# Optimization experiments

Measured on AMD Instinct MI355X. Metric: run time of the kernel, lower is better.

The kernel has to match this reference:

```python
import jax, jax.numpy as jnp
import numpy as np

N_DNA = 220000   # multiple of 11 (11 pseudo-atoms per base-pair)
N_PROT = 120000
E = 1500000
C = 32           # prot_channels == dna_channels
IN = C + 4 + C   # [x_prot_j, ppf(4), x_dna_i]

BRANCH_MODS = [(0, 10), (1, 9), (2, 3, 4, 5), (6, 7, 8)]  # p, s, M, m edge groups


def setup_inputs() -> dict:
    key = jax.random.key(0)
    ks = jax.random.split(key, 10)
    return {
        "x_dna": jax.random.normal(ks[0], (N_DNA, C), jnp.float32),
        "v_dna": jax.random.normal(ks[1], (N_DNA, 3), jnp.float32),
        "x_prot": jax.random.normal(ks[2], (N_PROT, C), jnp.float32),
        "v_prot": jax.random.normal(ks[3], (N_PROT, 3), jnp.float32),
        "prot_vec": jax.random.normal(ks[4], (N_PROT, 3), jnp.float32),
        "dna_vec": jax.random.normal(ks[5], (N_DNA, 3), jnp.float32),
        "edge_src": jax.random.randint(ks[6], (E,), 0, N_PROT),
        "edge_dst": jax.random.randint(ks[7], (E,), 0, N_DNA),
        "W1": jax.random.normal(ks[8], (4, IN, C), jnp.float32) / np.sqrt(IN).astype(np.float32),
        "b1": jnp.zeros((4, C), jnp.float32),
        "W2": jax.random.normal(ks[9], (4, C, C), jnp.float32) / np.sqrt(C).astype(np.float32),
        "b2": jnp.zeros((4, C), jnp.float32),
    }


def _angle(v1, v2):
    cross = jnp.cross(v1, v2)
    return jnp.arctan2(jnp.linalg.norm(cross, axis=-1), jnp.sum(v1 * v2, axis=-1))


def _point_pair_features(pos_i, pos_j, n_i, n_j):
    d = pos_j - pos_i
    return jnp.stack([
        jnp.linalg.norm(d, axis=-1),
        _angle(n_i, d),
        _angle(n_j, d),
        _angle(n_i, n_j),
    ], axis=-1)  # [E, 4]


def reference(x_dna, v_dna, x_prot, v_prot, prot_vec, dna_vec,
              edge_src, edge_dst, W1, b1, W2, b2):
    n_dna, c = x_dna.shape
    # PPF: i = target (dna), j = source (prot)
    ppf = _point_pair_features(v_dna[edge_dst], v_prot[edge_src],
                               dna_vec[edge_dst], prot_vec[edge_src])
    # per-edge input features, add_target_features=True concatenates x_dna_i
    feat = jnp.concatenate([x_prot[edge_src], ppf, x_dna[edge_dst]], axis=-1)  # [E, IN]
    mod = edge_dst % 11
    out = jnp.zeros_like(x_dna)
    conv = jnp.zeros_like(x_dna)
    for b, mods in enumerate(BRANCH_MODS):
        mask = jnp.zeros(mod.shape, dtype=bool)
        for m in mods:
            mask = mask | (mod == m)
        h = jax.nn.relu(feat @ W1[b] + b1[b])
        h = jax.nn.relu(h @ W2[b] + b2[b])          # [E, C] per-edge messages
        agg = jax.ops.segment_sum(jnp.where(mask[:, None], h, 0.0),
                                  edge_dst, num_segments=n_dna)
        conv = conv + agg
        out = out + jax.nn.relu(agg)
    return out.reshape(-1, 11, c), conv
```

## Files before the change

### kernel.cpp

```cpp
#include <hip/hip_runtime.h>


#define IN_C 32
#define IN_F 68
#define TILE_A 4096
#define BK_SHIFT 9
#define NBKT_MAX 448
#define BCAP 6144

using bf16x8v = __attribute__((ext_vector_type(8))) short;
using f32x16v = __attribute__((ext_vector_type(16))) float;
using f32x2v  = __attribute__((ext_vector_type(2))) float;

union U4F { unsigned u[4]; bf16x8v v; };

__device__ __forceinline__ unsigned cvtpk_bf16(float a, float b) {
    unsigned r;
    asm("v_cvt_pk_bf16_f32 %0, %1, %2" : "=v"(r) : "v"(a), "v"(b));
    return r;
}
__device__ __forceinline__ float bflo(unsigned u) { return __uint_as_float(u << 16); }
__device__ __forceinline__ float bfhi(unsigned u) { return __uint_as_float(u & 0xffff0000u); }

__device__ __forceinline__ float angf(float ax, float ay, float az,
                                      float bx, float by, float bz) {
    float cx = ay * bz - az * by;
    float cy = az * bx - ax * bz;
    float cz = ax * by - ay * bx;
    float cn = sqrtf(cx * cx + cy * cy + cz * cz);
    float dt = ax * bx + ay * by + az * bz;
    return atan2f(cn, dt);
}

__device__ __forceinline__ int branch_of(int m) {
    if (m == 0 || m == 10) return 0;
    if (m == 1 || m == 9)  return 1;
    if (m >= 2 && m <= 5)  return 2;
    return 3;
}

__device__ __forceinline__ unsigned bf16r(float f) {
    unsigned u = __float_as_uint(f);
    return (u + 0x7fffu + ((u >> 16) & 1u)) >> 16;
}

__device__ __forceinline__ void precomp_body_fast(
    int t,
    const float* __restrict__ x_prot, const float* __restrict__ x_dna,
    const float* __restrict__ v_prot, const float* __restrict__ prot_vec,
    const float* __restrict__ v_dna, const float* __restrict__ dna_vec,
    const float* __restrict__ W1, const float* __restrict__ b1,
    int NP, int NPpad, int NB, int NBpad,
    unsigned* __restrict__ yrec, unsigned* __restrict__ drec)
{
    float h[IN_C];
    if (t < NPpad) {
        int p = t;
        if (p >= NP) return;
        float xs[IN_C];
        {
            const float4* xp = reinterpret_cast<const float4*>(x_prot + (size_t)p * IN_C);
            #pragma unroll
            for (int kk = 0; kk < 8; ++kk) {
                float4 xv = xp[kk];
                xs[4 * kk + 0] = xv.x; xs[4 * kk + 1] = xv.y;
                xs[4 * kk + 2] = xv.z; xs[4 * kk + 3] = xv.w;
            }
        }
        float vpx = v_prot[p * 3 + 0], vpy = v_prot[p * 3 + 1], vpz = v_prot[p * 3 + 2];
        float njx = prot_vec[p * 3 + 0], njy = prot_vec[p * 3 + 1], njz = prot_vec[p * 3 + 2];
        uint4 gr;
        gr.x = bf16r(vpx) | (bf16r(vpy) << 16);
        gr.y = bf16r(vpz) | (bf16r(njx) << 16);
        gr.z = bf16r(njy) | (bf16r(njz) << 16);
        gr.w = 0;
        #pragma unroll 1
        for (int g = 0; g < 4; ++g) {
            const float* Wa = W1 + g * (IN_F * IN_C);
            #pragma unroll
            for (int c = 0; c < IN_C; ++c) h[c] = 0.0f;
            #pragma unroll
            for (int k = 0; k < IN_C; ++k)
                #pragma unroll
                for (int c = 0; c < IN_C; ++c)
                    h[c] = fmaf(xs[k], Wa[k * IN_C + c], h[c]);
            unsigned yw[8];
            #pragma unroll
            for (int j = 0; j < 8; ++j) {
                int w = 0;
                w = __builtin_amdgcn_cvt_pk_fp8_f32(h[4 * j],     h[4 * j + 1], w, false);
                w = __builtin_amdgcn_cvt_pk_fp8_f32(h[4 * j + 2], h[4 * j + 3], w, true);
                yw[j] = (unsigned)w;
            }
            uint4* d4 = reinterpret_cast<uint4*>(yrec + ((size_t)g * NP + p) * 16);
            d4[0] = make_uint4(yw[0], yw[1], yw[2], yw[3]);
            d4[1] = make_uint4(yw[4], yw[5], yw[6], yw[7]);
            d4[2] = gr;
        }
    } else {
        int t2 = t - NPpad;
        int q = t2 / NBpad;
        if (q >= 11) return;
        int idx = t2 - q * NBpad;
        if (idx >= NB) return;
        int g, m;
        if (q < 2)      { g = 0; m = q ? 10 : 0; }
        else if (q < 4) { g = 1; m = (q == 2) ? 1 : 9; }
        else if (q < 8) { g = 2; m = 2 + (q - 4); }
        else            { g = 3; m = 6 + (q - 8); }
        int bb = __builtin_amdgcn_readfirstlane(g);
        int dn = idx * 11 + m;
        const float* Wa = W1 + bb * (IN_F * IN_C);
        const float* ba = b1 + bb * IN_C;
        #pragma unroll
        for (int c = 0; c < IN_C; ++c) h[c] = ba[c];
        const float4* xd = reinterpret_cast<const float4*>(x_dna + (size_t)dn * IN_C);
        #pragma unroll
        for (int kk = 0; kk < 8; ++kk) {
            float4 xv = xd[kk];
            float fs[4] = {xv.x, xv.y, xv.z, xv.w};
            #pragma unroll
            for (int j = 0; j < 4; ++j)
                #pragma unroll
                for (int c = 0; c < IN_C; ++c)
                    h[c] = fmaf(fs[j], Wa[(36 + kk * 4 + j) * IN_C + c], h[c]);
        }
        unsigned yw[16];
        #pragma unroll
        for (int j = 0; j < 16; ++j)
            yw[j] = bf16r(h[2 * j]) | (bf16r(h[2 * j + 1]) << 16);
        float vdx = v_dna[dn * 3 + 0], vdy = v_dna[dn * 3 + 1], vdz = v_dna[dn * 3 + 2];
        float nix = dna_vec[dn * 3 + 0], niy = dna_vec[dn * 3 + 1], niz = dna_vec[dn * 3 + 2];
        uint4 gr;
        gr.x = bf16r(vdx) | (bf16r(vdy) << 16);
        gr.y = bf16r(vdz) | (bf16r(nix) << 16);
        gr.z = bf16r(niy) | (bf16r(niz) << 16);
        gr.w = 0;
        uint4* d4 = reinterpret_cast<uint4*>(drec + (size_t)dn * 32);
        d4[0] = make_uint4(yw[0],  yw[1],  yw[2],  yw[3]);
        d4[1] = make_uint4(yw[4],  yw[5],  yw[6],  yw[7]);
        d4[2] = make_uint4(yw[8],  yw[9],  yw[10], yw[11]);
        d4[3] = make_uint4(yw[12], yw[13], yw[14], yw[15]);
        d4[4] = gr;
    }
}

__global__ __launch_bounds__(256) void k_passA(
    const int* __restrict__ esrc, const int* __restrict__ edst, int E,
    int nbkt, int* __restrict__ gcur, unsigned* __restrict__ stage)
{
    __shared__ unsigned rec[TILE_A];
    __shared__ unsigned short bkt[TILE_A];
    __shared__ int hist[NBKT_MAX];
    __shared__ int hscan[NBKT_MAX];
    __shared__ int cnt[NBKT_MAX];
    __shared__ int gpos[NBKT_MAX];
    __shared__ int chbase[8];

    int base = blockIdx.x * TILE_A;
    int n = E - base; if (n > TILE_A) n = TILE_A;
    if (n <= 0) return;

    for (int i = threadIdx.x; i < nbkt; i += 256) hist[i] = 0;
    __syncthreads();

    unsigned myrec[16];
    int mybkt[16];
    #pragma unroll
    for (int k = 0; k < 16; ++k) {
        int i = threadIdx.x + k * 256;
        mybkt[k] = -1;
        if (i < n) {
            int s = esrc[base + i];
            int d = edst[base + i];
            int b = d >> BK_SHIFT;
            myrec[k] = ((unsigned)(d & ((1 << BK_SHIFT) - 1)) << 17) | (unsigned)s;
            mybkt[k] = b;
            atomicAdd(&hist[b], 1);
        }
    }
    __syncthreads();

    {
        int lane = threadIdx.x & 63, w = threadIdx.x >> 6;
        int nch = (nbkt + 63) >> 6;
        for (int ch = w; ch < nch; ch += 4) {
            int idx = (ch << 6) + lane;
            int v = (idx < nbkt) ? hist[idx] : 0;
            int inc = v;
            #pragma unroll
            for (int d = 1; d < 64; d <<= 1) {
                int u = __shfl_up(inc, d, 64);
                if (lane >= d) inc += u;
            }
            if (idx < nbkt) hscan[idx] = inc - v;
            if (lane == 63) chbase[ch] = inc;
        }
        __syncthreads();
        if (threadIdx.x == 0) {
            int s = 0;
            for (int ch = 0; ch < nch; ++ch) { int t2 = chbase[ch]; chbase[ch] = s; s += t2; }
        }
        __syncthreads();
        for (int i = threadIdx.x; i < nbkt; i += 256) {
            int v = hscan[i] + chbase[i >> 6];
            hscan[i] = v;
            cnt[i] = v;
        }
    }
    for (int b2 = threadIdx.x; b2 < nbkt; b2 += 256) {
        int c = hist[b2];
        if (c > 0) gpos[b2] = b2 * BCAP + atomicAdd(&gcur[b2], c);
    }
    __syncthreads();

    #pragma unroll
    for (int k = 0; k < 16; ++k) {
        if (mybkt[k] >= 0) {
            int p = atomicAdd(&cnt[mybkt[k]], 1);
            rec[p] = myrec[k];
            bkt[p] = (unsigned short)mybkt[k];
        }
    }
    __syncthreads();

    for (int i = threadIdx.x; i < n; i += 256) {
        int b2 = bkt[i];
        stage[gpos[b2] + (i - hscan[b2])] = rec[i];
    }
}

__global__ __launch_bounds__(256) void k_passB2(
    const unsigned* __restrict__ stage, const int* __restrict__ gcur,
    int nbkt, int ND,
    int* __restrict__ counts, int* __restrict__ rowend,
    int* __restrict__ pool_src, int* __restrict__ hist)
{
    __shared__ int lcnt[512];
    __shared__ int lpre[512];
    __shared__ int lh[256];
    __shared__ int wsum[4];
    __shared__ int spp[4];
    __shared__ int s_pstart;

    int b = blockIdx.x;

    {
        int partial = 0;
        for (int i = threadIdx.x; i < b; i += 256) partial += gcur[i];
        #pragma unroll
        for (int d = 1; d < 64; d <<= 1) partial += __shfl_xor(partial, d, 64);
        int lane = threadIdx.x & 63, w = threadIdx.x >> 6;
        if (lane == 0) spp[w] = partial;
    }
    lcnt[threadIdx.x] = 0;
    lcnt[threadIdx.x + 256] = 0;
    lh[threadIdx.x] = 0;
    __syncthreads();
    if (threadIdx.x == 0) s_pstart = spp[0] + spp[1] + spp[2] + spp[3];
    __syncthreads();

    int cnt = gcur[b];
    int pstart = s_pstart;
    int dbase = b << BK_SHIFT;

    for (int i = threadIdx.x; i < cnt; i += 256)
        atomicAdd(&lcnt[stage[(size_t)b * BCAP + i] >> 17], 1);
    __syncthreads();

    int e0 = lcnt[2 * threadIdx.x], e1 = lcnt[2 * threadIdx.x + 1];
    int s = e0 + e1;
    int lane = threadIdx.x & 63, w = threadIdx.x >> 6;
    int inc = s;
    #pragma unroll
    for (int d = 1; d < 64; d <<= 1) {
        int u = __shfl_up(inc, d, 64);
        if (lane >= d) inc += u;
    }
    if (lane == 63) wsum[w] = inc;
    __syncthreads();
    if (threadIdx.x == 0) {
        int a = 0;
        #pragma unroll
        for (int g = 0; g < 4; ++g) { int tmp = wsum[g]; wsum[g] = a; a += tmp; }
    }
    __syncthreads();
    int excl = inc - s + wsum[w];
    lpre[2 * threadIdx.x]     = excl;
    lpre[2 * threadIdx.x + 1] = excl + e0;

    #pragma unroll
    for (int k = 0; k < 2; ++k) {
        int nid = 2 * threadIdx.x + k;
        int node = dbase + nid;
        if (node < ND) {
            int c = lcnt[nid];
            counts[node] = c;
            rowend[node] = pstart + lpre[nid] + c;
            int cc = c > 63 ? 63 : c;
            atomicAdd(&lh[branch_of(node % 11) * 64 + (63 - cc)], 1);
        }
    }
    __syncthreads();
    if (lh[threadIdx.x]) atomicAdd(&hist[threadIdx.x], lh[threadIdx.x]);

    for (int i = threadIdx.x; i < cnt; i += 256) {
        unsigned r = stage[(size_t)b * BCAP + i];
        int nid = r >> 17;
        int pos = atomicAdd(&lpre[nid], 1);
        pool_src[pstart + pos] = (int)(r & 0x1FFFFu);
    }
}

__global__ __launch_bounds__(256) void k_tail(
    const int* __restrict__ counts, const int* __restrict__ hist,
    int* __restrict__ cur, int* __restrict__ pbs,
    int* __restrict__ node_order, int ND, int nbA,
    const float* __restrict__ x_prot, const float* __restrict__ x_dna,
    const float* __restrict__ v_prot, const float* __restrict__ prot_vec,
    const float* __restrict__ v_dna, const float* __restrict__ dna_vec,
    const float* __restrict__ W1, const float* __restrict__ b1,
    int NP, int NPpad, int NB, int NBpad,
    unsigned* __restrict__ yrec, unsigned* __restrict__ drec)
{
    if ((int)blockIdx.x >= nbA) {
        int t = (blockIdx.x - nbA) * 256 + threadIdx.x;
        precomp_body_fast(t, x_prot, x_dna, v_prot, prot_vec, v_dna, dna_vec,
                          W1, b1, NP, NPpad, NB, NBpad, yrec, drec);
        return;
    }

    __shared__ int sh_scan[256];
    __shared__ int sh_gb[5];
    __shared__ int sh_ge[4];
    __shared__ int gsum[4];
    __shared__ int lh[256];
    __shared__ int lbase[256];

    int lane = threadIdx.x & 63;
    int w = threadIdx.x >> 6;
    int v = hist[threadIdx.x];
    int inc = v;
    #pragma unroll
    for (int d = 1; d < 64; d <<= 1) {
        int u = __shfl_up(inc, d, 64);
        if (lane >= d) inc += u;
    }
    if (lane == 63) gsum[w] = inc;
    lh[threadIdx.x] = 0;
    __syncthreads();
    if (threadIdx.x == 0) {
        int base = 0;
        #pragma unroll
        for (int g = 0; g < 4; ++g) {
            sh_gb[g] = base;
            sh_ge[g] = base + gsum[g];
            base = (base + gsum[g] + 31) & ~31;
        }
        sh_gb[4] = base;
    }
    __syncthreads();
    sh_scan[threadIdx.x] = sh_gb[w] + inc - v;
    __syncthreads();

    int t = blockIdx.x * 256 + threadIdx.x;
    bool vld = (t < ND);
    int bin = 0, rank = 0;
    if (vld) {
        int g = branch_of(t % 11);
        int c = counts[t]; c = c > 63 ? 63 : c;
        bin = g * 64 + (63 - c);
        rank = atomicAdd(&lh[bin], 1);
    }
    __syncthreads();
    int cnt = lh[threadIdx.x];
    if (cnt > 0) lbase[threadIdx.x] = atomicAdd(&cur[threadIdx.x], cnt);
    __syncthreads();
    if (vld) node_order[sh_scan[bin] + lbase[bin] + rank] = t;

    if (blockIdx.x == 0) {
        if (threadIdx.x < 5) pbs[threadIdx.x] = sh_gb[threadIdx.x];
        if (threadIdx.x < 128) {
            int g = threadIdx.x >> 5, k = threadIdx.x & 31;
            int pos = sh_ge[g] + k;
            if (pos < sh_gb[g + 1]) node_order[pos] = -1;
        }
    }
}

__global__ void k_count(const int* __restrict__ edst, int E, int* counts) {
    int t = blockIdx.x * blockDim.x + threadIdx.x;
    if (t >= E) return;
    atomicAdd(&counts[edst[t]], 1);
}

__global__ __launch_bounds__(1024) void k_scan1(const int* __restrict__ counts,
                                                int NN, int NDp, int* cursor,
                                                int* blk, int* hist,
                                                int* node_order) {
    __shared__ int wsum[16];
    __shared__ int lh[256];
    if (threadIdx.x < 256) lh[threadIdx.x] = 0;
    __syncthreads();
    int t = blockIdx.x * 1024 + threadIdx.x;
    int lane = threadIdx.x & 63;
    int wid = threadIdx.x >> 6;
    int c = (t < NN) ? counts[t] : 0;
    if (t < NN) {
        int g = branch_of(t % 11);
        int cc = c > 63 ? 63 : c;
        atomicAdd(&lh[g * 64 + (63 - cc)], 1);
    }
    if (t < NDp) node_order[t] = -1;
    int inc = c;
    #pragma unroll
    for (int d = 1; d < 64; d <<= 1) {
        int v = __shfl_up(inc, d, 64);
        if (lane >= d) inc += v;
    }
    if (lane == 63) wsum[wid] = inc;
    __syncthreads();
    if (threadIdx.x < 16) {
        int v = wsum[threadIdx.x];
        int wi = v;
        #pragma unroll
        for (int d = 1; d < 16; d <<= 1) {
            int u = __shfl_up(wi, d, 64);
            if (threadIdx.x >= d) wi += u;
        }
        wsum[threadIdx.x] = wi - v;
        if (threadIdx.x == 15) blk[blockIdx.x] = wi;
    }
    __syncthreads();
    if (t < NN) cursor[t] = inc - c + wsum[wid];
    if (threadIdx.x < 256 && lh[threadIdx.x])
        atomicAdd(&hist[threadIdx.x], lh[threadIdx.x]);
}

__global__ __launch_bounds__(256) void k_scan2(int* blk, int nblk) {
    __shared__ int wsum[4];
    int lane = threadIdx.x & 63;
    int wid = threadIdx.x >> 6;
    int v = (threadIdx.x < nblk) ? blk[threadIdx.x] : 0;
    int inc = v;
    #pragma unroll
    for (int d = 1; d < 64; d <<= 1) {
        int u = __shfl_up(inc, d, 64);
        if (lane >= d) inc += u;
    }
    if (lane == 63) wsum[wid] = inc;
    __syncthreads();
    if (threadIdx.x < 4) {
        int w = wsum[threadIdx.x];
        int wi = w;
        #pragma unroll
        for (int d = 1; d < 4; d <<= 1) {
            int u = __shfl_up(wi, d, 64);
            if (threadIdx.x >= d) wi += u;
        }
        wsum[threadIdx.x] = wi - w;
    }
    __syncthreads();
    if (threadIdx.x < nblk) blk[threadIdx.x] = inc - v + wsum[wid];
}

__global__ __launch_bounds__(1024) void k_scan3(int* cursor, const int* blk, int NN) {
    int t = blockIdx.x * 1024 + threadIdx.x;
    if (t >= NN) return;
    cursor[t] += blk[blockIdx.x];
}

__global__ void k_fill(const int* __restrict__ esrc, const int* __restrict__ edst,
                       int E, int* cursor, int* __restrict__ pool_src) {
    int t = blockIdx.x * blockDim.x + threadIdx.x;
    if (t >= E) return;
    int pos = atomicAdd(&cursor[edst[t]], 1);
    pool_src[pos] = esrc[t];
}

__global__ __launch_bounds__(256) void k_padscan2(int* hist, int* pbs) {
    __shared__ int gsum[4];
    __shared__ int gbase[5];
    int lane = threadIdx.x & 63;
    int w = threadIdx.x >> 6;
    int v = hist[threadIdx.x];
    int inc = v;
    #pragma unroll
    for (int d = 1; d < 64; d <<= 1) {
        int u = __shfl_up(inc, d, 64);
        if (lane >= d) inc += u;
    }
    if (lane == 63) gsum[w] = inc;
    __syncthreads();
    if (threadIdx.x == 0) {
        int base = 0;
        #pragma unroll
        for (int g = 0; g < 4; ++g) {
            gbase[g] = base;
            base = (base + gsum[g] + 31) & ~31;
        }
        gbase[4] = base;
    }
    __syncthreads();
    hist[threadIdx.x] = gbase[w] + inc - v;
    if (threadIdx.x < 5) pbs[threadIdx.x] = gbase[threadIdx.x];
}

__global__ __launch_bounds__(256) void k_assign(const int* __restrict__ counts,
                                                int ND, int* cur,
                                                int* __restrict__ node_order) {
    __shared__ int lh[256];
    __shared__ int lbase[256];
    lh[threadIdx.x] = 0;
    __syncthreads();
    int t = blockIdx.x * 256 + threadIdx.x;
    bool v = (t < ND);
    int bin = 0, rank = 0;
    if (v) {
        int g = branch_of(t % 11);
        int c = counts[t]; c = c > 63 ? 63 : c;
        bin = g * 64 + (63 - c);
        rank = atomicAdd(&lh[bin], 1);
    }
    __syncthreads();
    int cnt = lh[threadIdx.x];
    if (cnt > 0) lbase[threadIdx.x] = atomicAdd(&cur[threadIdx.x], cnt);
    __syncthreads();
    if (v) node_order[lbase[bin] + rank] = t;
}

__global__ __launch_bounds__(256) void k_precomp1(
    const float* __restrict__ x_prot, const float* __restrict__ W1,
    int NP, int NPpad, unsigned short* __restrict__ ypb)
{
    int t = blockIdx.x * 256 + threadIdx.x;
    int g = t / NPpad;
    int p = t - g * NPpad;
    if (g > 3 || p >= NP) return;
    int bb = __builtin_amdgcn_readfirstlane(g);
    const float* Wa = W1 + bb * (IN_F * IN_C);
    float h[IN_C];
    #pragma unroll
    for (int c = 0; c < IN_C; ++c) h[c] = 0.0f;
    const float4* xp = reinterpret_cast<const float4*>(x_prot + (size_t)p * IN_C);
    #pragma unroll
    for (int kk = 0; kk < 8; ++kk) {
        float4 xv = xp[kk];
        float fs[4] = {xv.x, xv.y, xv.z, xv.w};
        #pragma unroll
        for (int j = 0; j < 4; ++j)
            #pragma unroll
            for (int c = 0; c < IN_C; ++c)
                h[c] = fmaf(fs[j], Wa[(kk * 4 + j) * IN_C + c], h[c]);
    }
    unsigned yw[16];
    #pragma unroll
    for (int j = 0; j < 16; ++j)
        yw[j] = bf16r(h[2 * j]) | (bf16r(h[2 * j + 1]) << 16);
    uint4* d4 = reinterpret_cast<uint4*>(ypb + ((size_t)bb * NP + p) * IN_C);
    d4[0] = make_uint4(yw[0], yw[1], yw[2], yw[3]);
    d4[1] = make_uint4(yw[4], yw[5], yw[6], yw[7]);
    d4[2] = make_uint4(yw[8], yw[9], yw[10], yw[11]);
    d4[3] = make_uint4(yw[12], yw[13], yw[14], yw[15]);
}

__global__ __launch_bounds__(256) void k_mfma(
    const float* __restrict__ W1, const float* __restrict__ W2,
    const float* __restrict__ b2,
    const int* __restrict__ node_order, const int* __restrict__ rowend,
    const int* __restrict__ counts, const int* __restrict__ pool_src,
    const int* __restrict__ pbs,
    const unsigned* __restrict__ yrec, const unsigned* __restrict__ drec,
    int NP, float* __restrict__ out, float* __restrict__ conv, int NDp)
{
    int nblk = gridDim.x;
    int q8 = nblk >> 3, r8 = nblk & 7;
    int x = blockIdx.x & 7, bidx = blockIdx.x >> 3;
    int lb = (x < r8 ? x * (q8 + 1) : r8 * (q8 + 1) + (x - r8) * q8) + bidx;

    int t = lb * 256 + threadIdx.x;
    int lane = threadIdx.x & 63;
    int hi = lane >> 5;
    int col = lane & 31;
    int pid = t >> 1;
    int sub = t & 1;

    int pb1 = pbs[1], pb2v = pbs[2], pb3 = pbs[3], pb4 = pbs[4];
    int g = (pid >= pb1) + (pid >= pb2v) + (pid >= pb3);
    int bb = __builtin_amdgcn_readfirstlane(g);

    int dst = (pid < pb4) ? node_order[pid] : -1;
    bool vnode = (dst >= 0);
    int dsafe = vnode ? dst : 0;
    int n_all = vnode ? counts[dsafe] : 0;
    int start = vnode ? (rowend[dsafe] - n_all) : 0;

    const float* Wp = W1 + bb * (IN_F * IN_C) + 32 * IN_C;
    const float* Wb = W2 + bb * (IN_C * IN_C);
    float b2c = b2[bb * IN_C + col];

    U4F B0u, B1u;
    #pragma unroll
    for (int j = 0; j < 4; ++j) {
        int k0 = hi * 8 + 2 * j;
        B0u.u[j] = cvtpk_bf16(Wb[k0 * IN_C + col],        Wb[(k0 + 1) * IN_C + col]);
        B1u.u[j] = cvtpk_bf16(Wb[(16 + k0) * IN_C + col], Wb[(17 + k0) * IN_C + col]);
    }

    unsigned ydw[16];
    float vdx, vdy, vdz, nix, niy, niz;
    {
        const uint4* dv = reinterpret_cast<const uint4*>(drec + (size_t)dsafe * 32);
        uint4 d0 = dv[0], d1 = dv[1], d2 = dv[2], d3 = dv[3], d4v = dv[4];
        *reinterpret_cast<uint4*>(&ydw[0])  = d0;
        *reinterpret_cast<uint4*>(&ydw[4])  = d1;
        *reinterpret_cast<uint4*>(&ydw[8])  = d2;
        *reinterpret_cast<uint4*>(&ydw[12]) = d3;
        vdx = bflo(d4v.x); vdy = bfhi(d4v.x);
        vdz = bflo(d4v.y); nix = bfhi(d4v.y);
        niy = bflo(d4v.z); niz = bfhi(d4v.z);
    }

    float acc[16];
    #pragma unroll
    for (int i = 0; i < 16; ++i) acc[i] = 0.0f;

    int niter = (n_all + 1) >> 1;
    #pragma unroll
    for (int d = 1; d < 64; d <<= 1) {
        int o = __shfl_xor(niter, d, 64);
        niter = niter > o ? niter : o;
    }

    unsigned ywc[8];
    unsigned gwc[4];
    if (niter > 0) {
        bool v0 = vnode && (sub < n_all);
        int off0 = v0 ? (start + sub) : 0;
        int src0 = pool_src[off0];
        const uint4* yv = reinterpret_cast<const uint4*>(yrec + ((size_t)bb * NP + src0) * 16);
        uint4 y0 = yv[0], y1 = yv[1], g2 = yv[2];
        *reinterpret_cast<uint4*>(&ywc[0]) = y0;
        *reinterpret_cast<uint4*>(&ywc[4]) = y1;
        *reinterpret_cast<uint4*>(&gwc[0]) = g2;
    }

    for (int it = 0; it < niter; ++it) {
        bool valid = vnode && (2 * it + sub < n_all);
        unsigned long long vm = __ballot(valid);

        int it1 = it + 1;
        bool vn = (it1 < niter) && vnode && (2 * it1 + sub < n_all);
        int offn = vn ? (start + 2 * it1 + sub) : 0;
        int src_n = pool_src[offn];
        const uint4* yvn = reinterpret_cast<const uint4*>(yrec + ((size_t)bb * NP + src_n) * 16);
        uint4 n0 = yvn[0], n1 = yvn[1], n2 = yvn[2];

        float vpx = bflo(gwc[0]), vpy = bfhi(gwc[0]);
        float vpz = bflo(gwc[1]), njx = bfhi(gwc[1]);
        float njy = bflo(gwc[2]), njz = bfhi(gwc[2]);
        float dx = vpx - vdx, dy = vpy - vdy, dz = vpz - vdz;
        float pf0 = sqrtf(dx * dx + dy * dy + dz * dz);
        float pf1 = angf(nix, niy, niz, dx, dy, dz);
        float pf2 = angf(njx, njy, njz, dx, dy, dz);
        float pf3 = angf(nix, niy, niz, njx, njy, njz);

        unsigned p[16];
        #pragma unroll
        for (int jj = 0; jj < 8; ++jj) {
            f32x2v f01 = __builtin_amdgcn_cvt_pk_f32_fp8((int)ywc[jj], false);
            f32x2v f23 = __builtin_amdgcn_cvt_pk_f32_fp8((int)ywc[jj], true);
            int c0 = 4 * jj;
            float a0 = bflo(ydw[2 * jj])     + f01[0];
            float a1 = bfhi(ydw[2 * jj])     + f01[1];
            float a2 = bflo(ydw[2 * jj + 1]) + f23[0];
            float a3 = bfhi(ydw[2 * jj + 1]) + f23[1];
            a0 = fmaf(pf0, Wp[0 * IN_C + c0],     a0);
            a0 = fmaf(pf1, Wp[1 * IN_C + c0],     a0);
            a0 = fmaf(pf2, Wp[2 * IN_C + c0],     a0);
            a0 = fmaf(pf3, Wp[3 * IN_C + c0],     a0);
            a1 = fmaf(pf0, Wp[0 * IN_C + c0 + 1], a1);
            a1 = fmaf(pf1, Wp[1 * IN_C + c0 + 1], a1);
            a1 = fmaf(pf2, Wp[2 * IN_C + c0 + 1], a1);
            a1 = fmaf(pf3, Wp[3 * IN_C + c0 + 1], a1);
            a2 = fmaf(pf0, Wp[0 * IN_C + c0 + 2], a2);
            a2 = fmaf(pf1, Wp[1 * IN_C + c0 + 2], a2);
            a2 = fmaf(pf2, Wp[2 * IN_C + c0 + 2], a2);
            a2 = fmaf(pf3, Wp[3 * IN_C + c0 + 2], a2);
            a3 = fmaf(pf0, Wp[0 * IN_C + c0 + 3], a3);
            a3 = fmaf(pf1, Wp[1 * IN_C + c0 + 3], a3);
            a3 = fmaf(pf2, Wp[2 * IN_C + c0 + 3], a3);
            a3 = fmaf(pf3, Wp[3 * IN_C + c0 + 3], a3);
            p[2 * jj]     = cvtpk_bf16(fmaxf(a0, 0.0f), fmaxf(a1, 0.0f));
            p[2 * jj + 1] = cvtpk_bf16(fmaxf(a2, 0.0f), fmaxf(a3, 0.0f));
        }

        unsigned q[16];
        #pragma unroll
        for (int j = 0; j < 16; ++j)
            q[j] = (unsigned)__shfl_xor((int)p[j], 32, 64);

        U4F a00, a01, a10, a11;
        #pragma unroll
        for (int d2 = 0; d2 < 4; ++d2) {
            a00.u[d2] = hi ? q[4 + d2]  : p[d2];
            a01.u[d2] = hi ? q[12 + d2] : p[8 + d2];
            a10.u[d2] = hi ? p[4 + d2]  : q[d2];
            a11.u[d2] = hi ? p[12 + d2] : q[8 + d2];
        }

        unsigned long long vms = vm >> (4 * hi);

        {
            f32x16v D;
            #pragma unroll
            for (int r = 0; r < 16; ++r) D[r] = 0.0f;
            D = __builtin_amdgcn_mfma_f32_32x32x16_bf16(a00.v, B0u.v, D, 0, 0, 0);
            D = __builtin_amdgcn_mfma_f32_32x32x16_bf16(a01.v, B1u.v, D, 0, 0, 0);
            #pragma unroll
            for (int r = 0; r < 16; ++r) {
                int sh = (r & 3) + 8 * (r >> 2);
                float val = fmaxf(D[r] + b2c, 0.0f);
                bool ok = (vms >> sh) & 1ull;
                int ai = 2 * (r >> 2) + ((r & 3) >> 1);
                acc[ai] += ok ? val : 0.0f;
            }
        }
        {
            f32x16v D;
            #pragma unroll
            for (int r = 0; r < 16; ++r) D[r] = 0.0f;
            D = __builtin_amdgcn_mfma_f32_32x32x16_bf16(a10.v, B0u.v, D, 0, 0, 0);
            D = __builtin_amdgcn_mfma_f32_32x32x16_bf16(a11.v, B1u.v, D, 0, 0, 0);
            #pragma unroll
            for (int r = 0; r < 16; ++r) {
                int sh = 32 + (r & 3) + 8 * (r >> 2);
                float val = fmaxf(D[r] + b2c, 0.0f);
                bool ok = (vms >> sh) & 1ull;
                int ai = 8 + 2 * (r >> 2) + ((r & 3) >> 1);
                acc[ai] += ok ? val : 0.0f;
            }
        }

        *reinterpret_cast<uint4*>(&ywc[0]) = n0;
        *reinterpret_cast<uint4*>(&ywc[4]) = n1;
        *reinterpret_cast<uint4*>(&gwc[0]) = n2;
    }

    #pragma unroll
    for (int i = 0; i < 16; ++i) {
        int rb = i >> 3, rem = i & 7;
        int q2 = rem >> 1, u = rem & 1;
        int m = 16 * rb + 4 * q2 + 2 * hi + u;
        int dm = __shfl(dst, 2 * m, 64);
        if (dm >= 0) {
            out[(size_t)dm * IN_C + col]  = acc[i];
            conv[(size_t)dm * IN_C + col] = acc[i];
        }
    }
}

template <int MODE>
__global__ __launch_bounds__(256) void k_nodes4(
    const float* __restrict__ x_dna, const float* __restrict__ v_dna,
    const float* __restrict__ x_prot, const float* __restrict__ v_prot,
    const float* __restrict__ prot_vec, const float* __restrict__ dna_vec,
    const float* __restrict__ W1, const float* __restrict__ b1,
    const float* __restrict__ W2, const float* __restrict__ b2,
    const int* __restrict__ node_order, const int* __restrict__ rowend,
    const int* __restrict__ counts, const int* __restrict__ pool_src,
    const int* __restrict__ pbs,
    const unsigned short* __restrict__ yp,
    int NP, float* __restrict__ out, float* __restrict__ conv, int NDp)
{
    int t = blockIdx.x * 256 + threadIdx.x;
    int pid = t >> 2;
    int sub = t & 3;
    if (pid >= NDp) return;

    int pb1 = pbs[1], pb2 = pbs[2], pb3 = pbs[3];
    int g = (pid >= pb1) + (pid >= pb2) + (pid >= pb3);
    int bb = __builtin_amdgcn_readfirstlane(g);

    int dst = node_order[pid];
    bool valid = (dst >= 0);
    int dsafe = valid ? dst : 0;

    int n_all = valid ? counts[dsafe] : 0;
    int start_all = valid ? (rowend[dsafe] - n_all) : 0;
    int nb4 = n_all >> 2, rem = n_all & 3;
    int n = nb4 + (sub < rem ? 1 : 0);
    int start = start_all + sub * nb4 + (sub < rem ? sub : rem);

    const float* Wa  = W1 + bb * (IN_F * IN_C);
    const float* Wp  = Wa + 32 * IN_C;
    const float* Wb  = W2 + bb * (IN_C * IN_C);
    const float* ba  = b1 + bb * IN_C;
    const float* bb2 = b2 + bb * IN_C;

    float vdx = v_dna[dsafe * 3 + 0], vdy = v_dna[dsafe * 3 + 1], vdz = v_dna[dsafe * 3 + 2];
    float nix = dna_vec[dsafe * 3 + 0], niy = dna_vec[dsafe * 3 + 1], niz = dna_vec[dsafe * 3 + 2];

    float h1b[IN_C];
    #pragma unroll
    for (int c = 0; c < IN_C; ++c) h1b[c] = ba[c];
    {
        const float4* xd = reinterpret_cast<const float4*>(x_dna + (size_t)dsafe * IN_C);
        #pragma unroll
        for (int kk = 0; kk < 8; ++kk) {
            float4 xv = xd[kk];
            float fs[4] = {xv.x, xv.y, xv.z, xv.w};
            #pragma unroll
            for (int j = 0; j < 4; ++j)
                #pragma unroll
                for (int c = 0; c < IN_C; ++c)
                    h1b[c] = fmaf(fs[j], Wa[(36 + kk * 4 + j) * IN_C + c], h1b[c]);
        }
    }

    float acc[IN_C];
    #pragma unroll
    for (int c = 0; c < IN_C; ++c) acc[c] = 0.0f;

    for (int k = 0; k < n; ++k) {
        int src = pool_src[start + k];
        float vpx = v_prot[src * 3 + 0], vpy = v_prot[src * 3 + 1], vpz = v_prot[src * 3 + 2];
        float njx = prot_vec[src * 3 + 0], njy = prot_vec[src * 3 + 1], njz = prot_vec[src * 3 + 2];
        float dx = vpx - vdx, dy = vpy - vdy, dz = vpz - vdz;
        float pf0 = sqrtf(dx * dx + dy * dy + dz * dz);
        float pf1 = angf(nix, niy, niz, dx, dy, dz);
        float pf2 = angf(njx, njy, njz, dx, dy, dz);
        float pf3 = angf(nix, niy, niz, njx, njy, njz);

        float h2[IN_C];
        #pragma unroll
        for (int c = 0; c < IN_C; ++c) h2[c] = bb2[c];

        if constexpr (MODE == 1) {
            unsigned yw[16];
            const uint4* ypv = reinterpret_cast<const uint4*>(yp + ((size_t)bb * NP + src) * IN_C);
            uint4 y0 = ypv[0], y1 = ypv[1], y2 = ypv[2], y3 = ypv[3];
            *reinterpret_cast<uint4*>(&yw[0])  = y0;
            *reinterpret_cast<uint4*>(&yw[4])  = y1;
            *reinterpret_cast<uint4*>(&yw[8])  = y2;
            *reinterpret_cast<uint4*>(&yw[12]) = y3;
            #pragma unroll
            for (int k2 = 0; k2 < IN_C; ++k2) {
                unsigned w = yw[k2 >> 1];
                float ypf = (k2 & 1) ? bfhi(w) : bflo(w);
                float h1v = h1b[k2] + ypf;
                h1v = fmaf(pf0, Wp[0 * IN_C + k2], h1v);
                h1v = fmaf(pf1, Wp[1 * IN_C + k2], h1v);
                h1v = fmaf(pf2, Wp[2 * IN_C + k2], h1v);
                h1v = fmaf(pf3, Wp[3 * IN_C + k2], h1v);
                float f = fmaxf(h1v, 0.0f);
                #pragma unroll
                for (int c = 0; c < IN_C; ++c)
                    h2[c] = fmaf(f, Wb[k2 * IN_C + c], h2[c]);
            }
        } else {
            float pf[4] = {pf0, pf1, pf2, pf3};
            const float4* xp = reinterpret_cast<const float4*>(x_prot + (size_t)src * IN_C);
            #pragma unroll
            for (int hh = 0; hh < 2; ++hh) {
                float h1h[16];
                #pragma unroll
                for (int c = 0; c < 16; ++c) h1h[c] = h1b[hh * 16 + c];
                #pragma unroll
                for (int kk = 0; kk < 8; ++kk) {
                    float4 xv = xp[kk];
                    float fs[4] = {xv.x, xv.y, xv.z, xv.w};
                    #pragma unroll
                    for (int j = 0; j < 4; ++j)
                        #pragma unroll
                        for (int c = 0; c < 16; ++c)
                            h1h[c] = fmaf(fs[j], Wa[(kk * 4 + j) * IN_C + hh * 16 + c], h1h[c]);
                }
                #pragma unroll
                for (int j = 0; j < 4; ++j)
                    #pragma unroll
                    for (int c = 0; c < 16; ++c)
                        h1h[c] = fmaf(pf[j], Wp[j * IN_C + hh * 16 + c], h1h[c]);
                #pragma unroll
                for (int k2 = 0; k2 < 16; ++k2) {
                    float f = fmaxf(h1h[k2], 0.0f);
                    #pragma unroll
                    for (int c = 0; c < IN_C; ++c)
                        h2[c] = fmaf(f, Wb[(hh * 16 + k2) * IN_C + c], h2[c]);
                }
            }
        }

        #pragma unroll
        for (int c = 0; c < IN_C; ++c)
            acc[c] += fmaxf(h2[c], 0.0f);
    }

    #pragma unroll
    for (int c = 0; c < IN_C; ++c)
        acc[c] += __shfl_xor(acc[c], 1, 64);
    #pragma unroll
    for (int c = 0; c < IN_C; ++c)
        acc[c] += __shfl_xor(acc[c], 2, 64);

    if (valid && sub < 2) {
        float* p = (sub ? conv : out) + (size_t)dst * IN_C;
        float4* p4 = reinterpret_cast<float4*>(p);
        #pragma unroll
        for (int qq = 0; qq < 8; ++qq) {
            float4 v;
            v.x = acc[qq * 4 + 0]; v.y = acc[qq * 4 + 1];
            v.z = acc[qq * 4 + 2]; v.w = acc[qq * 4 + 3];
            p4[qq] = v;
        }
    }
}

__global__ __launch_bounds__(256) void k_edges_fallback(
    const float* __restrict__ x_dna, const float* __restrict__ v_dna,
    const float* __restrict__ x_prot, const float* __restrict__ v_prot,
    const float* __restrict__ prot_vec, const float* __restrict__ dna_vec,
    const int* __restrict__ esrc, const int* __restrict__ edst,
    const float* __restrict__ W1, const float* __restrict__ b1,
    const float* __restrict__ W2, const float* __restrict__ b2,
    int E, float* __restrict__ conv)
{
    int t = blockIdx.x * blockDim.x + threadIdx.x;
    if (t >= E) return;
    int src = esrc[t], dst = edst[t];
    int b = branch_of(dst % 11);
    const float* Wa  = W1 + b * (IN_F * IN_C);
    const float* Wb  = W2 + b * (IN_C * IN_C);
    const float* ba  = b1 + b * IN_C;
    const float* bb2 = b2 + b * IN_C;

    float vdx = v_dna[dst * 3 + 0], vdy = v_dna[dst * 3 + 1], vdz = v_dna[dst * 3 + 2];
    float vpx = v_prot[src * 3 + 0], vpy = v_prot[src * 3 + 1], vpz = v_prot[src * 3 + 2];
    float nix = dna_vec[dst * 3 + 0], niy = dna_vec[dst * 3 + 1], niz = dna_vec[dst * 3 + 2];
    float njx = prot_vec[src * 3 + 0], njy = prot_vec[src * 3 + 1], njz = prot_vec[src * 3 + 2];
    float dx = vpx - vdx, dy = vpy - vdy, dz = vpz - vdz;
    float pf[4];
    pf[0] = sqrtf(dx * dx + dy * dy + dz * dz);
    pf[1] = angf(nix, niy, niz, dx, dy, dz);
    pf[2] = angf(njx, njy, njz, dx, dy, dz);
    pf[3] = angf(nix, niy, niz, njx, njy, njz);

    float h1[IN_C];
    #pragma unroll
    for (int c = 0; c < IN_C; ++c) h1[c] = ba[c];
    const float4* xp = reinterpret_cast<const float4*>(x_prot + (size_t)src * IN_C);
    #pragma unroll
    for (int kk = 0; kk < 8; ++kk) {
        float4 xv = xp[kk];
        float fs[4] = {xv.x, xv.y, xv.z, xv.w};
        #pragma unroll
        for (int j = 0; j < 4; ++j)
            #pragma unroll
            for (int c = 0; c < IN_C; ++c)
                h1[c] = fmaf(fs[j], Wa[(kk * 4 + j) * IN_C + c], h1[c]);
    }
    #pragma unroll
    for (int j = 0; j < 4; ++j)
        #pragma unroll
        for (int c = 0; c < IN_C; ++c)
            h1[c] = fmaf(pf[j], Wa[(32 + j) * IN_C + c], h1[c]);
    const float4* xd = reinterpret_cast<const float4*>(x_dna + (size_t)dst * IN_C);
    #pragma unroll
    for (int kk = 0; kk < 8; ++kk) {
        float4 xv = xd[kk];
        float fs[4] = {xv.x, xv.y, xv.z, xv.w};
        #pragma unroll
        for (int j = 0; j < 4; ++j)
            #pragma unroll
            for (int c = 0; c < IN_C; ++c)
                h1[c] = fmaf(fs[j], Wa[(36 + kk * 4 + j) * IN_C + c], h1[c]);
    }
    float h2[IN_C];
    #pragma unroll
    for (int c = 0; c < IN_C; ++c) h2[c] = bb2[c];
    #pragma unroll
    for (int k = 0; k < IN_C; ++k) {
        float f = fmaxf(h1[k], 0.0f);
        #pragma unroll
        for (int c = 0; c < IN_C; ++c)
            h2[c] = fmaf(f, Wb[k * IN_C + c], h2[c]);
    }
    float* cv = conv + (size_t)dst * IN_C;
    #pragma unroll
    for (int c = 0; c < IN_C; ++c)
        atomicAdd(&cv[c], fmaxf(h2[c], 0.0f));
}

extern "C" void kernel_launch(void* const* d_in, const int* in_sizes, int n_in,
                              void* d_out, int out_size, void* d_ws, size_t ws_size,
                              hipStream_t stream) {
    const float* x_dna    = (const float*)d_in[0];
    const float* v_dna    = (const float*)d_in[1];
    const float* x_prot   = (const float*)d_in[2];
    const float* v_prot   = (const float*)d_in[3];
    const float* prot_vec = (const float*)d_in[4];
    const float* dna_vec  = (const float*)d_in[5];
    const int*   esrc     = (const int*)d_in[6];
    const int*   edst     = (const int*)d_in[7];
    const float* W1       = (const float*)d_in[8];
    const float* b1       = (const float*)d_in[9];
    const float* W2       = (const float*)d_in[10];
    const float* b2       = (const float*)d_in[11];

    const int E  = in_sizes[6];
    const int ND = in_sizes[0] / IN_C;
    const int NP = in_sizes[2] / IN_C;
    const int half = out_size / 2;
    float* out  = (float*)d_out;
    float* conv = out + half;

    const int NDp = (ND + 160 + 31) & ~31;
    const int nblk_scan = (NDp + 1023) / 1024;
    const int eb = (E + 255) / 256;

    const size_t base_ints = (size_t)ND + 256 + 512 + 256 + 16 + 256 + ND + NDp + E;
    const size_t ws_base   = base_ints * sizeof(int);
    const size_t yp_off    = (ws_base + 255) & ~(size_t)255;
    const size_t yrec_bytes = (size_t)NP * 4 * 64;
    const size_t ypb_bytes  = (size_t)NP * 4 * IN_C * 2;
    const size_t yd_off    = yp_off + yrec_bytes;
    const size_t yd_bytes  = (size_t)ND * 128;

    if (ND == half / IN_C && ws_size >= ws_base && nblk_scan <= 256) {
        int* counts     = (int*)d_ws;
        int* hist       = counts + ND;
        int* gcur       = hist + 256;
        int* cur        = gcur + 512;
        int* pbs        = cur + 256;
        int* blk        = pbs + 16;
        int* rowcur     = blk + 256;
        int* node_order = rowcur + ND;
        int* pool_src   = node_order + NDp;
        unsigned*       yrec = (unsigned*)((char*)d_ws + yp_off);
        unsigned short* ypb  = (unsigned short*)((char*)d_ws + yp_off);
        unsigned*       drec = (unsigned*)((char*)d_ws + yd_off);

        int mode = 0;
        if (ws_size >= yd_off + yd_bytes && ND % 11 == 0) mode = 2;
        else if (ws_size >= yp_off + ypb_bytes)           mode = 1;

        const int nbkt = (ND + (1 << BK_SHIFT) - 1) >> BK_SHIFT;
        const size_t stage_bytes = (size_t)nbkt * BCAP * sizeof(unsigned);
        const bool fastfill = (mode == 2) && (NP < (1 << 17)) && (nbkt <= NBKT_MAX)
                              && (stage_bytes <= yrec_bytes)
                              && (E / nbkt + 512 < BCAP);
        if (mode == 2 && !fastfill)
            mode = (ws_size >= yp_off + ypb_bytes) ? 1 : 0;

        int NPpad = (NP + 63) & ~63;
        int NB = ND / 11;
        int NBpad = (NB + 63) & ~63;

        if (mode == 2) {
            unsigned* stage = yrec;
            hipMemsetAsync(hist, 0, 1024 * sizeof(int), stream);
            int na = (E + TILE_A - 1) / TILE_A;
            k_passA<<<na, 256, 0, stream>>>(esrc, edst, E, nbkt, gcur, stage);
            k_passB2<<<nbkt, 256, 0, stream>>>(stage, gcur, nbkt, ND,
                                               counts, rowcur, pool_src, hist);
            int nbA = (ND + 255) / 256;
            int totP = NPpad + 11 * NBpad;
            int nbP = (totP + 255) / 256;
            k_tail<<<nbA + nbP, 256, 0, stream>>>(
                counts, hist, cur, pbs, node_order, ND, nbA,
                x_prot, x_dna, v_prot, prot_vec, v_dna, dna_vec, W1, b1,
                NP, NPpad, NB, NBpad, yrec, drec);

            int nbm = (2 * NDp + 255) / 256;
            k_mfma<<<nbm, 256, 0, stream>>>(
                W1, W2, b2, node_order, rowcur, counts, pool_src, pbs,
                yrec, drec, NP, out, conv, NDp);
        } else {
            hipMemsetAsync(counts, 0, ((size_t)ND + 256) * sizeof(int), stream);
            k_count<<<eb, 256, 0, stream>>>(edst, E, counts);
            k_scan1<<<nblk_scan, 1024, 0, stream>>>(counts, ND, NDp, rowcur, blk,
                                                    hist, node_order);
            k_scan2<<<1, 256, 0, stream>>>(blk, nblk_scan);
            k_scan3<<<nblk_scan, 1024, 0, stream>>>(rowcur, blk, ND);
            k_fill<<<eb, 256, 0, stream>>>(esrc, edst, E, rowcur, pool_src);
            k_padscan2<<<1, 256, 0, stream>>>(hist, pbs);
            k_assign<<<(ND + 255) / 256, 256, 0, stream>>>(counts, ND, hist,
                                                           node_order);
            if (mode == 1) {
                int tot = 4 * NPpad;
                k_precomp1<<<(tot + 255) / 256, 256, 0, stream>>>(
                    x_prot, W1, NP, NPpad, ypb);
                int nb4 = (4 * NDp + 255) / 256;
                k_nodes4<1><<<nb4, 256, 0, stream>>>(
                    x_dna, v_dna, x_prot, v_prot, prot_vec, dna_vec,
                    W1, b1, W2, b2, node_order, rowcur, counts, pool_src, pbs,
                    ypb, NP, out, conv, NDp);
            } else {
                int nb4 = (4 * NDp + 255) / 256;
                k_nodes4<0><<<nb4, 256, 0, stream>>>(
                    x_dna, v_dna, x_prot, v_prot, prot_vec, dna_vec,
                    W1, b1, W2, b2, node_order, rowcur, counts, pool_src, pbs,
                    nullptr, NP, out, conv, NDp);
            }
        }
    } else {
        hipMemsetAsync(conv, 0, (size_t)half * sizeof(float), stream);
        k_edges_fallback<<<eb, 256, 0, stream>>>(
            x_dna, v_dna, x_prot, v_prot, prot_vec, dna_vec,
            esrc, edst, W1, b1, W2, b2, E, conv);
        hipMemcpyAsync(out, conv, (size_t)half * sizeof(float),
                       hipMemcpyDeviceToDevice, stream);
    }
}
```

Before: 158.2 us.

## Move protein-side projection into edge bucketing pass and stage buckets in drec buffer

The per-protein W1 projection (fp8 yrec records) now runs as extra blocks of the first edge-bucketing kernel instead of in the tail kernel. This lets that projection overlap with the bucketing pass and leaves the tail kernel with only the DNA-side projection. Because yrec is now written while bucketing is still running, the staging buffer is moved from yrec to drec, and the fast-path size check now tests against drec's size. The change depends on drec not being written until passB2 has finished reading the stage buffer.

After: 158.5 us. About the same (+0.2%).

```diff
diff --git a/kernel.cpp b/kernel.cpp
--- a/kernel.cpp
+++ b/kernel.cpp
@@ -44,18 +44,23 @@
     return (u + 0x7fffu + ((u >> 16) & 1u)) >> 16;
 }
 
-__device__ __forceinline__ void precomp_body_fast(
-    int t,
-    const float* __restrict__ x_prot, const float* __restrict__ x_dna,
-    const float* __restrict__ v_prot, const float* __restrict__ prot_vec,
-    const float* __restrict__ v_dna, const float* __restrict__ dna_vec,
-    const float* __restrict__ W1, const float* __restrict__ b1,
-    int NP, int NPpad, int NB, int NBpad,
-    unsigned* __restrict__ yrec, unsigned* __restrict__ drec)
+__global__ __launch_bounds__(256) void k_passA_fused(
+    const int* __restrict__ esrc, const int* __restrict__ edst, int E,
+    int nbkt, int* __restrict__ gcur, unsigned* __restrict__ stage, int na,
+    const float* __restrict__ x_prot, const float* __restrict__ v_prot,
+    const float* __restrict__ prot_vec, const float* __restrict__ W1,
+    int NP, unsigned* __restrict__ yrec)
 {
-    float h[IN_C];
-    if (t < NPpad) {
-        int p = t;
+    __shared__ unsigned rec[TILE_A];
+    __shared__ unsigned short bkt[TILE_A];
+    __shared__ int hist[NBKT_MAX];
+    __shared__ int hscan[NBKT_MAX];
+    __shared__ int cnt[NBKT_MAX];
+    __shared__ int gpos[NBKT_MAX];
+    __shared__ int chbase[8];
+
+    if ((int)blockIdx.x >= na) {
+        int p = (blockIdx.x - na) * 256 + threadIdx.x;
         if (p >= NP) return;
         float xs[IN_C];
         {
@@ -74,6 +79,7 @@
         gr.y = bf16r(vpz) | (bf16r(njx) << 16);
         gr.z = bf16r(njy) | (bf16r(njz) << 16);
         gr.w = 0;
+        float h[IN_C];
         #pragma unroll 1
         for (int g = 0; g < 4; ++g) {
             const float* Wa = W1 + g * (IN_F * IN_C);
@@ -97,8 +103,175 @@
             d4[1] = make_uint4(yw[4], yw[5], yw[6], yw[7]);
             d4[2] = gr;
         }
-    } else {
-        int t2 = t - NPpad;
+        return;
+    }
+
+    int base = blockIdx.x * TILE_A;
+    int n = E - base; if (n > TILE_A) n = TILE_A;
+    if (n <= 0) return;
+
+    for (int i = threadIdx.x; i < nbkt; i += 256) hist[i] = 0;
+    __syncthreads();
+
+    unsigned myrec[16];
+    int mybkt[16];
+    #pragma unroll
+    for (int k = 0; k < 16; ++k) {
+        int i = threadIdx.x + k * 256;
+        mybkt[k] = -1;
+        if (i < n) {
+            int s = esrc[base + i];
+            int d = edst[base + i];
+            int b = d >> BK_SHIFT;
+            myrec[k] = ((unsigned)(d & ((1 << BK_SHIFT) - 1)) << 17) | (unsigned)s;
+            mybkt[k] = b;
+            atomicAdd(&hist[b], 1);
+        }
+    }
+    __syncthreads();
+
+    {
+        int lane = threadIdx.x & 63, w = threadIdx.x >> 6;
+        int nch = (nbkt + 63) >> 6;
+        for (int ch = w; ch < nch; ch += 4) {
+            int idx = (ch << 6) + lane;
+            int v = (idx < nbkt) ? hist[idx] : 0;
+            int inc = v;
+            #pragma unroll
+            for (int d = 1; d < 64; d <<= 1) {
+                int u = __shfl_up(inc, d, 64);
+                if (lane >= d) inc += u;
+            }
+            if (idx < nbkt) hscan[idx] = inc - v;
+            if (lane == 63) chbase[ch] = inc;
+        }
+        __syncthreads();
+        if (threadIdx.x == 0) {
+            int s = 0;
+            for (int ch = 0; ch < nch; ++ch) { int t2 = chbase[ch]; chbase[ch] = s; s += t2; }
+        }
+        __syncthreads();
+        for (int i = threadIdx.x; i < nbkt; i += 256) {
+            int v = hscan[i] + chbase[i >> 6];
+            hscan[i] = v;
+            cnt[i] = v;
+        }
+    }
+    for (int b2 = threadIdx.x; b2 < nbkt; b2 += 256) {
+        int c = hist[b2];
+        if (c > 0) gpos[b2] = b2 * BCAP + atomicAdd(&gcur[b2], c);
+    }
+    __syncthreads();
+
+    #pragma unroll
+    for (int k = 0; k < 16; ++k) {
+        if (mybkt[k] >= 0) {
+            int p = atomicAdd(&cnt[mybkt[k]], 1);
+            rec[p] = myrec[k];
+            bkt[p] = (unsigned short)mybkt[k];
+        }
+    }
+    __syncthreads();
+
+    for (int i = threadIdx.x; i < n; i += 256) {
+        int b2 = bkt[i];
+        stage[gpos[b2] + (i - hscan[b2])] = rec[i];
+    }
+}
+
+__global__ __launch_bounds__(256) void k_passB2(
+    const unsigned* __restrict__ stage, const int* __restrict__ gcur,
+    int nbkt, int ND,
+    int* __restrict__ counts, int* __restrict__ rowend,
+    int* __restrict__ pool_src, int* __restrict__ hist)
+{
+    __shared__ int lcnt[512];
+    __shared__ int lpre[512];
+    __shared__ int lh[256];
+    __shared__ int wsum[4];
+    __shared__ int spp[4];
+    __shared__ int s_pstart;
+
+    int b = blockIdx.x;
+
+    {
+        int partial = 0;
+        for (int i = threadIdx.x; i < b; i += 256) partial += gcur[i];
+        #pragma unroll
+        for (int d = 1; d < 64; d <<= 1) partial += __shfl_xor(partial, d, 64);
+        int lane = threadIdx.x & 63, w = threadIdx.x >> 6;
+        if (lane == 0) spp[w] = partial;
+    }
+    lcnt[threadIdx.x] = 0;
+    lcnt[threadIdx.x + 256] = 0;
+    lh[threadIdx.x] = 0;
+    __syncthreads();
+    if (threadIdx.x == 0) s_pstart = spp[0] + spp[1] + spp[2] + spp[3];
+    __syncthreads();
+
+    int cnt = gcur[b];
+    int pstart = s_pstart;
+    int dbase = b << BK_SHIFT;
+
+    for (int i = threadIdx.x; i < cnt; i += 256)
+        atomicAdd(&lcnt[stage[(size_t)b * BCAP + i] >> 17], 1);
+    __syncthreads();
+
+    int e0 = lcnt[2 * threadIdx.x], e1 = lcnt[2 * threadIdx.x + 1];
+    int s = e0 + e1;
+    int lane = threadIdx.x & 63, w = threadIdx.x >> 6;
+    int inc = s;
+    #pragma unroll
+    for (int d = 1; d < 64; d <<= 1) {
+        int u = __shfl_up(inc, d, 64);
+        if (lane >= d) inc += u;
+    }
+    if (lane == 63) wsum[w] = inc;
+    __syncthreads();
+    if (threadIdx.x == 0) {
+        int a = 0;
+        #pragma unroll
+        for (int g = 0; g < 4; ++g) { int tmp = wsum[g]; wsum[g] = a; a += tmp; }
+    }
+    __syncthreads();
+    int excl = inc - s + wsum[w];
+    lpre[2 * threadIdx.x]     = excl;
+    lpre[2 * threadIdx.x + 1] = excl + e0;
+
+    #pragma unroll
+    for (int k = 0; k < 2; ++k) {
+        int nid = 2 * threadIdx.x + k;
+        int node = dbase + nid;
+        if (node < ND) {
+            int c = lcnt[nid];
+            counts[node] = c;
+            rowend[node] = pstart + lpre[nid] + c;
+            int cc = c > 63 ? 63 : c;
+            atomicAdd(&lh[branch_of(node % 11) * 64 + (63 - cc)], 1);
+        }
+    }
+    __syncthreads();
+    if (lh[threadIdx.x]) atomicAdd(&hist[threadIdx.x], lh[threadIdx.x]);
+
+    for (int i = threadIdx.x; i < cnt; i += 256) {
+        unsigned r = stage[(size_t)b * BCAP + i];
+        int nid = r >> 17;
+        int pos = atomicAdd(&lpre[nid], 1);
+        pool_src[pstart + pos] = (int)(r & 0x1FFFFu);
+    }
+}
+
+__global__ __launch_bounds__(256) void k_tail(
+    const int* __restrict__ counts, const int* __restrict__ hist,
+    int* __restrict__ cur, int* __restrict__ pbs,
+    int* __restrict__ node_order, int ND, int nbA,
+    const float* __restrict__ x_dna,
+    const float* __restrict__ v_dna, const float* __restrict__ dna_vec,
+    const float* __restrict__ W1, const float* __restrict__ b1,
+    int NB, int NBpad, unsigned* __restrict__ drec)
+{
+    if ((int)blockIdx.x >= nbA) {
+        int t2 = (blockIdx.x - nbA) * 256 + threadIdx.x;
         int q = t2 / NBpad;
         if (q >= 11) return;
         int idx = t2 - q * NBpad;
@@ -112,6 +285,7 @@
         int dn = idx * 11 + m;
         const float* Wa = W1 + bb * (IN_F * IN_C);
         const float* ba = b1 + bb * IN_C;
+        float h[IN_C];
         #pragma unroll
         for (int c = 0; c < IN_C; ++c) h[c] = ba[c];
         const float4* xd = reinterpret_cast<const float4*>(x_dna + (size_t)dn * IN_C);
@@ -142,191 +316,6 @@
         d4[2] = make_uint4(yw[8],  yw[9],  yw[10], yw[11]);
         d4[3] = make_uint4(yw[12], yw[13], yw[14], yw[15]);
         d4[4] = gr;
-    }
-}
-
-__global__ __launch_bounds__(256) void k_passA(
-    const int* __restrict__ esrc, const int* __restrict__ edst, int E,
-    int nbkt, int* __restrict__ gcur, unsigned* __restrict__ stage)
-{
-    __shared__ unsigned rec[TILE_A];
-    __shared__ unsigned short bkt[TILE_A];
-    __shared__ int hist[NBKT_MAX];
-    __shared__ int hscan[NBKT_MAX];
-    __shared__ int cnt[NBKT_MAX];
-    __shared__ int gpos[NBKT_MAX];
-    __shared__ int chbase[8];
-
-    int base = blockIdx.x * TILE_A;
-    int n = E - base; if (n > TILE_A) n = TILE_A;
-    if (n <= 0) return;
-
-    for (int i = threadIdx.x; i < nbkt; i += 256) hist[i] = 0;
-    __syncthreads();
-
-    unsigned myrec[16];
-    int mybkt[16];
-    #pragma unroll
-    for (int k = 0; k < 16; ++k) {
-        int i = threadIdx.x + k * 256;
-        mybkt[k] = -1;
-        if (i < n) {
-            int s = esrc[base + i];
-            int d = edst[base + i];
-            int b = d >> BK_SHIFT;
-            myrec[k] = ((unsigned)(d & ((1 << BK_SHIFT) - 1)) << 17) | (unsigned)s;
-            mybkt[k] = b;
-            atomicAdd(&hist[b], 1);
-        }
-    }
-    __syncthreads();
-
-    {
-        int lane = threadIdx.x & 63, w = threadIdx.x >> 6;
-        int nch = (nbkt + 63) >> 6;
-        for (int ch = w; ch < nch; ch += 4) {
-            int idx = (ch << 6) + lane;
-            int v = (idx < nbkt) ? hist[idx] : 0;
-            int inc = v;
-            #pragma unroll
-            for (int d = 1; d < 64; d <<= 1) {
-                int u = __shfl_up(inc, d, 64);
-                if (lane >= d) inc += u;
-            }
-            if (idx < nbkt) hscan[idx] = inc - v;
-            if (lane == 63) chbase[ch] = inc;
-        }
-        __syncthreads();
-        if (threadIdx.x == 0) {
-            int s = 0;
-            for (int ch = 0; ch < nch; ++ch) { int t2 = chbase[ch]; chbase[ch] = s; s += t2; }
-        }
-        __syncthreads();
-        for (int i = threadIdx.x; i < nbkt; i += 256) {
-            int v = hscan[i] + chbase[i >> 6];
-            hscan[i] = v;
-            cnt[i] = v;
-        }
-    }
-    for (int b2 = threadIdx.x; b2 < nbkt; b2 += 256) {
-        int c = hist[b2];
-        if (c > 0) gpos[b2] = b2 * BCAP + atomicAdd(&gcur[b2], c);
-    }
-    __syncthreads();
-
-    #pragma unroll
-    for (int k = 0; k < 16; ++k) {
-        if (mybkt[k] >= 0) {
-            int p = atomicAdd(&cnt[mybkt[k]], 1);
-            rec[p] = myrec[k];
-            bkt[p] = (unsigned short)mybkt[k];
-        }
-    }
-    __syncthreads();
-
-    for (int i = threadIdx.x; i < n; i += 256) {
-        int b2 = bkt[i];
-        stage[gpos[b2] + (i - hscan[b2])] = rec[i];
-    }
-}
-
-__global__ __launch_bounds__(256) void k_passB2(
-    const unsigned* __restrict__ stage, const int* __restrict__ gcur,
-    int nbkt, int ND,
-    int* __restrict__ counts, int* __restrict__ rowend,
-    int* __restrict__ pool_src, int* __restrict__ hist)
-{
-    __shared__ int lcnt[512];
-    __shared__ int lpre[512];
-    __shared__ int lh[256];
-    __shared__ int wsum[4];
-    __shared__ int spp[4];
-    __shared__ int s_pstart;
-
-    int b = blockIdx.x;
-
-    {
-        int partial = 0;
-        for (int i = threadIdx.x; i < b; i += 256) partial += gcur[i];
-        #pragma unroll
-        for (int d = 1; d < 64; d <<= 1) partial += __shfl_xor(partial, d, 64);
-        int lane = threadIdx.x & 63, w = threadIdx.x >> 6;
-        if (lane == 0) spp[w] = partial;
-    }
-    lcnt[threadIdx.x] = 0;
-    lcnt[threadIdx.x + 256] = 0;
-    lh[threadIdx.x] = 0;
-    __syncthreads();
-    if (threadIdx.x == 0) s_pstart = spp[0] + spp[1] + spp[2] + spp[3];
-    __syncthreads();
-
-    int cnt = gcur[b];
-    int pstart = s_pstart;
-    int dbase = b << BK_SHIFT;
-
-    for (int i = threadIdx.x; i < cnt; i += 256)
-        atomicAdd(&lcnt[stage[(size_t)b * BCAP + i] >> 17], 1);
-    __syncthreads();
-
-    int e0 = lcnt[2 * threadIdx.x], e1 = lcnt[2 * threadIdx.x + 1];
-    int s = e0 + e1;
-    int lane = threadIdx.x & 63, w = threadIdx.x >> 6;
-    int inc = s;
-    #pragma unroll
-    for (int d = 1; d < 64; d <<= 1) {
-        int u = __shfl_up(inc, d, 64);
-        if (lane >= d) inc += u;
-    }
-    if (lane == 63) wsum[w] = inc;
-    __syncthreads();
-    if (threadIdx.x == 0) {
-        int a = 0;
-        #pragma unroll
-        for (int g = 0; g < 4; ++g) { int tmp = wsum[g]; wsum[g] = a; a += tmp; }
-    }
-    __syncthreads();
-    int excl = inc - s + wsum[w];
-    lpre[2 * threadIdx.x]     = excl;
-    lpre[2 * threadIdx.x + 1] = excl + e0;
-
-    #pragma unroll
-    for (int k = 0; k < 2; ++k) {
-        int nid = 2 * threadIdx.x + k;
-        int node = dbase + nid;
-        if (node < ND) {
-            int c = lcnt[nid];
-            counts[node] = c;
-            rowend[node] = pstart + lpre[nid] + c;
-            int cc = c > 63 ? 63 : c;
-            atomicAdd(&lh[branch_of(node % 11) * 64 + (63 - cc)], 1);
-        }
-    }
-    __syncthreads();
-    if (lh[threadIdx.x]) atomicAdd(&hist[threadIdx.x], lh[threadIdx.x]);
-
-    for (int i = threadIdx.x; i < cnt; i += 256) {
-        unsigned r = stage[(size_t)b * BCAP + i];
-        int nid = r >> 17;
-        int pos = atomicAdd(&lpre[nid], 1);
-        pool_src[pstart + pos] = (int)(r & 0x1FFFFu);
-    }
-}
-
-__global__ __launch_bounds__(256) void k_tail(
-    const int* __restrict__ counts, const int* __restrict__ hist,
-    int* __restrict__ cur, int* __restrict__ pbs,
-    int* __restrict__ node_order, int ND, int nbA,
-    const float* __restrict__ x_prot, const float* __restrict__ x_dna,
-    const float* __restrict__ v_prot, const float* __restrict__ prot_vec,
-    const float* __restrict__ v_dna, const float* __restrict__ dna_vec,
-    const float* __restrict__ W1, const float* __restrict__ b1,
-    int NP, int NPpad, int NB, int NBpad,
-    unsigned* __restrict__ yrec, unsigned* __restrict__ drec)
-{
-    if ((int)blockIdx.x >= nbA) {
-        int t = (blockIdx.x - nbA) * 256 + threadIdx.x;
-        precomp_body_fast(t, x_prot, x_dna, v_prot, prot_vec, v_dna, dna_vec,
-                          W1, b1, NP, NPpad, NB, NBpad, yrec, drec);
         return;
     }
 
@@ -1047,7 +1036,7 @@
         const int nbkt = (ND + (1 << BK_SHIFT) - 1) >> BK_SHIFT;
         const size_t stage_bytes = (size_t)nbkt * BCAP * sizeof(unsigned);
         const bool fastfill = (mode == 2) && (NP < (1 << 17)) && (nbkt <= NBKT_MAX)
-                              && (stage_bytes <= yrec_bytes)
+                              && (stage_bytes <= yd_bytes)
                               && (E / nbkt + 512 < BCAP);
         if (mode == 2 && !fastfill)
             mode = (ws_size >= yp_off + ypb_bytes) ? 1 : 0;
@@ -1057,19 +1046,23 @@
         int NBpad = (NB + 63) & ~63;
 
         if (mode == 2) {
-            unsigned* stage = yrec;
+            unsigned* stage = drec;
             hipMemsetAsync(hist, 0, 1024 * sizeof(int), stream);
+
             int na = (E + TILE_A - 1) / TILE_A;
-            k_passA<<<na, 256, 0, stream>>>(esrc, edst, E, nbkt, gcur, stage);
+            int nbP = (NP + 255) / 256;
+            k_passA_fused<<<na + nbP, 256, 0, stream>>>(
+                esrc, edst, E, nbkt, gcur, stage, na,
+                x_prot, v_prot, prot_vec, W1, NP, yrec);
+
             k_passB2<<<nbkt, 256, 0, stream>>>(stage, gcur, nbkt, ND,
                                                counts, rowcur, pool_src, hist);
+
             int nbA = (ND + 255) / 256;
-            int totP = NPpad + 11 * NBpad;
-            int nbP = (totP + 255) / 256;
-            k_tail<<<nbA + nbP, 256, 0, stream>>>(
+            int nbD = (11 * NBpad + 255) / 256;
+            k_tail<<<nbA + nbD, 256, 0, stream>>>(
                 counts, hist, cur, pbs, node_order, ND, nbA,
-                x_prot, x_dna, v_prot, prot_vec, v_dna, dna_vec, W1, b1,
-                NP, NPpad, NB, NBpad, yrec, drec);
+                x_dna, v_dna, dna_vec, W1, b1, NB, NBpad, drec);
 
             int nbm = (2 * NDp + 255) / 256;
             k_mfma<<<nbm, 256, 0, stream>>>(
```
